# Kernel optimization log

Measured on AMD Instinct MI355X. Metric: run time of the kernel, lower is better.

The kernel has to match this reference:

```python
import jax, jax.numpy as jnp
import numpy as np

# Static graph-batch configuration (equal-size graphs so per-graph top-k is static)
B = 256          # number of graphs in the batch
N = 400          # nodes per graph
D = 256          # in_dim
DEG = 32         # average degree
E = B * N * DEG  # total edges
RATIO = 0.5
K = int(np.ceil(RATIO * N))  # nodes kept per graph by mytopk
NT = B * N


def setup_inputs() -> dict:
    key = jax.random.key(0)
    k1, k2, k3, k4 = jax.random.split(key, 4)
    feature = jax.random.normal(k1, (NT, D), dtype=jnp.float32)
    W = jax.random.normal(k2, (D, 1), dtype=jnp.float32) * (1.0 / np.sqrt(D))
    b = jnp.zeros((1,), dtype=jnp.float32)
    # edges stay within each graph: global id = graph_offset + local id
    g = jnp.repeat(jnp.arange(B, dtype=jnp.int32), N * DEG)  # [E] graph id per edge
    src = g * N + jax.random.randint(k3, (E,), 0, N, dtype=jnp.int32)
    dst = g * N + jax.random.randint(k4, (E,), 0, N, dtype=jnp.int32)
    return {"feature": feature, "W": W, "b": b, "src": src, "dst": dst}


def _forward(feature, W, b, src, dst):
    # --- GraphConv(in_dim, 1), norm='both' (dgl): h = D_in^-1/2 A D_out^-1/2 (X W) + b
    ones_e = jnp.ones((E,), dtype=feature.dtype)
    deg_out = jax.ops.segment_sum(ones_e, src, num_segments=NT)
    deg_in = jax.ops.segment_sum(ones_e, dst, num_segments=NT)
    norm_out = jnp.maximum(deg_out, 1.0) ** -0.5  # dgl clamps degree to min 1
    norm_in = jnp.maximum(deg_in, 1.0) ** -0.5
    h = (feature @ W) * norm_out[:, None]                      # [NT,1]
    agg = jax.ops.segment_sum(h[src], dst, num_segments=NT)    # [NT,1]
    score = (agg * norm_in[:, None] + b)[:, 0]                 # [NT]

    # --- mytopk: per-graph top-k node selection by score (descending)
    score2d = score.reshape(B, N)
    _, idx = jax.lax.top_k(score2d, K)                         # [B,K] local ids
    offsets = (jnp.arange(B, dtype=jnp.int32) * N)[:, None]
    perm = (idx.astype(jnp.int32) + offsets).reshape(-1)       # [B*K] global ids

    # complement nodes (mask trick in the original): ascending order per graph
    sel = jnp.zeros((NT,), dtype=bool).at[perm].set(True)
    sel2d = sel.reshape(B, N).astype(jnp.int32)
    order = jnp.argsort(sel2d, axis=1, stable=True)[:, : N - K]  # unselected first
    perm_com = (order.astype(jnp.int32) + offsets).reshape(-1)   # [B*(N-K)]

    # --- gated feature gathers
    feature_dis = feature[perm] * jnp.tanh(score[perm])[:, None]
    feature_com = feature[perm_com] * jnp.tanh(score[perm_com])[:, None]

    # --- subgraph structure as static-shape edge masks (dgl.node_subgraph keeps
    #     edges whose both endpoints are selected)
    e_dis_mask = sel[src] & sel[dst]
    e_com_mask = (~sel[src]) & (~sel[dst])

    score_soft = jax.nn.softmax(score, axis=0)  # Softmax(dim=0) over all nodes
    return feature_dis, feature_com, perm, perm_com, score_soft, e_dis_mask, e_com_mask


def reference(feature, W, b, src, dst):
    return _forward(feature, W, b, src, dst)
```

## Files before the change

kernel.cpp:

```cpp
#include <hip/hip_runtime.h>
#include <math.h>

#define B_    256
#define N_    400
#define D_    256
#define EPG_  12800
#define E_    3276800
#define NT_   102400
#define K_    200
#define NKC_  200

#define O_FDIS 0
#define O_FCOM 13107200
#define O_PERM 26214400
#define O_PCOM 26265600
#define O_SOFT 26316800
#define O_EDIS 26419200
#define O_ECOM 29696000

#define NEG_INF (-3.402823466e38f)

typedef float nfv4 __attribute__((ext_vector_type(4)));
static __device__ __forceinline__ void nt_store4(float4* p, float4 v) {
    nfv4 x; x.x = v.x; x.y = v.y; x.z = v.z; x.w = v.w;
    __builtin_nontemporal_store(x, (nfv4*)p);
}

__global__ __launch_bounds__(256) void k_h(const float* __restrict__ feat,
                                           const float* __restrict__ W,
                                           float* __restrict__ hraw,
                                           int* __restrict__ degz) {
    const int gid  = blockIdx.x * 256 + threadIdx.x;
    if (gid < 2 * NT_) degz[gid] = 0;
    const int gw   = gid >> 6;
    const int lane = threadIdx.x & 63;
    const float4 w4 = ((const float4*)W)[lane];
    const int r0 = gw * 4;
    const float4* fb = (const float4*)feat;
    float4 a0 = fb[(size_t)(r0    ) * 64 + lane];
    float4 a1 = fb[(size_t)(r0 + 1) * 64 + lane];
    float4 a2 = fb[(size_t)(r0 + 2) * 64 + lane];
    float4 a3 = fb[(size_t)(r0 + 3) * 64 + lane];
    float d0 = a0.x*w4.x + a0.y*w4.y + a0.z*w4.z + a0.w*w4.w;
    float d1 = a1.x*w4.x + a1.y*w4.y + a1.z*w4.z + a1.w*w4.w;
    float d2 = a2.x*w4.x + a2.y*w4.y + a2.z*w4.z + a2.w*w4.w;
    float d3 = a3.x*w4.x + a3.y*w4.y + a3.z*w4.z + a3.w*w4.w;
    #pragma unroll
    for (int off = 32; off > 0; off >>= 1) {
        d0 += __shfl_down(d0, off, 64);
        d1 += __shfl_down(d1, off, 64);
        d2 += __shfl_down(d2, off, 64);
        d3 += __shfl_down(d3, off, 64);
    }
    if (lane == 0) {
        hraw[r0    ] = d0;
        hraw[r0 + 1] = d1;
        hraw[r0 + 2] = d2;
        hraw[r0 + 3] = d3;
    }
}

__global__ __launch_bounds__(256) void k_deg(const int* __restrict__ src,
                                             const int* __restrict__ dst,
                                             int* __restrict__ dego,
                                             int* __restrict__ degi,
                                             float* __restrict__ aggz) {
    __shared__ int hp[8][N_];
    const int blk = blockIdx.x, tid = threadIdx.x, wave = tid >> 6;
    const int gid = blk * 256 + tid;
    if (gid < NT_) aggz[gid] = 0.0f;
    for (int t = tid; t < 8 * N_; t += 256) ((int*)hp)[t] = 0;
    __syncthreads();

    const int g = blk >> 2, nbase = g * N_;
    int* hw_o = hp[wave * 2 + 0];
    int* hw_i = hp[wave * 2 + 1];
    const int4* s4 = (const int4*)(src + blk * (EPG_ / 4));
    const int4* d4 = (const int4*)(dst + blk * (EPG_ / 4));
    for (int i = tid; i < EPG_ / 16; i += 256) {
        int4 s = s4[i]; int4 d = d4[i];
        atomicAdd(&hw_o[s.x - nbase], 1);
        atomicAdd(&hw_o[s.y - nbase], 1);
        atomicAdd(&hw_o[s.z - nbase], 1);
        atomicAdd(&hw_o[s.w - nbase], 1);
        atomicAdd(&hw_i[d.x - nbase], 1);
        atomicAdd(&hw_i[d.y - nbase], 1);
        atomicAdd(&hw_i[d.z - nbase], 1);
        atomicAdd(&hw_i[d.w - nbase], 1);
    }
    __syncthreads();
    for (int t = tid; t < N_; t += 256) {
        atomicAdd(&dego[nbase + t], hp[0][t] + hp[2][t] + hp[4][t] + hp[6][t]);
        atomicAdd(&degi[nbase + t], hp[1][t] + hp[3][t] + hp[5][t] + hp[7][t]);
    }
}

__global__ __launch_bounds__(256) void k_scat(const int* __restrict__ src,
                                              const int* __restrict__ dst,
                                              const float* __restrict__ hraw,
                                              const int* __restrict__ dego,
                                              float* __restrict__ agg) {
    __shared__ float hl[N_];
    __shared__ float sp[4][N_];
    const int blk = blockIdx.x, tid = threadIdx.x, wave = tid >> 6;
    const int g = blk >> 2, nbase = g * N_;
    for (int t = tid; t < N_; t += 256)
        hl[t] = hraw[nbase + t] * (1.0f / sqrtf(fmaxf((float)dego[nbase + t], 1.0f)));
    for (int t = tid; t < 4 * N_; t += 256) ((float*)sp)[t] = 0.0f;
    __syncthreads();

    float* spw = sp[wave];
    const int4* s4 = (const int4*)(src + blk * (EPG_ / 4));
    const int4* d4 = (const int4*)(dst + blk * (EPG_ / 4));
    for (int i = tid; i < EPG_ / 16; i += 256) {
        int4 s = s4[i]; int4 d = d4[i];
        atomicAdd(&spw[d.x - nbase], hl[s.x - nbase]);
        atomicAdd(&spw[d.y - nbase], hl[s.y - nbase]);
        atomicAdd(&spw[d.z - nbase], hl[s.z - nbase]);
        atomicAdd(&spw[d.w - nbase], hl[s.w - nbase]);
    }
    __syncthreads();
    for (int t = tid; t < N_; t += 256)
        atomicAdd(&agg[nbase + t], sp[0][t] + sp[1][t] + sp[2][t] + sp[3][t]);
}

__global__ __launch_bounds__(512) void k_top(float* __restrict__ sc,
                                             const int* __restrict__ degi,
                                             const float* __restrict__ bp,
                                             float* __restrict__ pm,
                                             float* __restrict__ ps,
                                             int* __restrict__ sel,
                                             int* __restrict__ orow,
                                             float* __restrict__ out) {
    __shared__ float scl[N_];
    __shared__ unsigned long long bmask[7];
    const int g = blockIdx.x, tid = threadIdx.x;
    const int wave = tid >> 6, lane = tid & 63;
    const int nbase = g * N_;

    const float bb = bp[0];
    if (tid < N_) {
        float v = sc[nbase + tid] * (1.0f / sqrtf(fmaxf((float)degi[nbase + tid], 1.0f))) + bb;
        sc[nbase + tid] = v;
        scl[tid] = v;
    }
    __syncthreads();

    bool selb = false;
    if (tid < 448) {
        float sreg[7];
        #pragma unroll
        for (int t = 0; t < 7; ++t) {
            const int j = t * 64 + lane;
            sreg[t] = (j < N_) ? scl[j] : NEG_INF;
        }
        const float v = (tid < N_) ? scl[tid] : NEG_INF;
        int rnk = 0;
        #pragma unroll
        for (int t = 0; t < 7; ++t) {
            #pragma unroll
            for (int l2 = 0; l2 < 64; ++l2) {
                const int j = t * 64 + l2;
                if (j < N_) {
                    const float u = __uint_as_float(
                        __builtin_amdgcn_readlane(__float_as_uint(sreg[t]), l2));
                    rnk += ((u > v) || (u == v && j < tid)) ? 1 : 0;
                }
            }
        }
        selb = (tid < N_) && (rnk < K_);
        if (tid < N_) sel[nbase + tid] = selb ? 1 : 0;
        if (selb) {
            orow[nbase + tid] = g * K_ + rnk;
            out[O_PERM + g * K_ + rnk] = (float)(nbase + tid);
        }
        unsigned long long bal = __ballot(selb);
        if (lane == 0) bmask[wave] = bal;
    }
    if (wave == 7) {
        float m = NEG_INF;
        for (int i = lane; i < N_; i += 64) m = fmaxf(m, scl[i]);
        #pragma unroll
        for (int o = 32; o > 0; o >>= 1) m = fmaxf(m, __shfl_xor(m, o, 64));
        float s = 0.0f;
        for (int i = lane; i < N_; i += 64) s += expf(scl[i] - m);
        #pragma unroll
        for (int o = 32; o > 0; o >>= 1) s += __shfl_xor(s, o, 64);
        if (lane == 0) { pm[g] = m; ps[g] = s; }
    }
    __syncthreads();

    if (tid < N_ && !selb) {
        int nsel = 0;
        #pragma unroll
        for (int w = 0; w < 7; ++w)
            if (w < wave) nsel += (int)__popcll(bmask[w]);
        nsel += (int)__popcll(bmask[wave] & ((1ull << lane) - 1ull));
        const int pos = tid - nsel;
        orow[nbase + tid] = B_ * K_ + g * NKC_ + pos;
        out[O_PCOM + g * NKC_ + pos] = (float)(nbase + tid);
    }
}

__global__ __launch_bounds__(256) void k_soft_comb(const float* pm, const float* ps, float* red2) {
    __shared__ float rm[256], rs[256];
    int tid = threadIdx.x;
    float m = pm[tid];
    rm[tid] = m; __syncthreads();
    for (int o = 128; o > 0; o >>= 1) { if (tid < o) rm[tid] = fmaxf(rm[tid], rm[tid + o]); __syncthreads(); }
    float M = rm[0]; __syncthreads();
    rs[tid] = ps[tid] * expf(m - M); __syncthreads();
    for (int o = 128; o > 0; o >>= 1) { if (tid < o) rs[tid] += rs[tid + o]; __syncthreads(); }
    if (tid == 0) { red2[0] = M; red2[1] = rs[0]; }
}

__global__ __launch_bounds__(256) void k_mask(const int* __restrict__ src,
                                              const int* __restrict__ dst,
                                              const int* __restrict__ sel,
                                              float* __restrict__ out) {
    const int i = blockIdx.x * 256 + threadIdx.x;
    int4 s = ((const int4*)src)[i];
    int4 d = ((const int4*)dst)[i];
    int a0 = sel[s.x], a1 = sel[s.y], a2 = sel[s.z], a3 = sel[s.w];
    int b0 = sel[d.x], b1 = sel[d.y], b2 = sel[d.z], b3 = sel[d.w];
    float4 mdis, mcom;
    mdis.x = (a0 & b0) ? 1.0f : 0.0f;  mcom.x = (a0 | b0) ? 0.0f : 1.0f;
    mdis.y = (a1 & b1) ? 1.0f : 0.0f;  mcom.y = (a1 | b1) ? 0.0f : 1.0f;
    mdis.z = (a2 & b2) ? 1.0f : 0.0f;  mcom.z = (a2 | b2) ? 0.0f : 1.0f;
    mdis.w = (a3 & b3) ? 1.0f : 0.0f;  mcom.w = (a3 | b3) ? 0.0f : 1.0f;
    nt_store4(((float4*)(out + O_EDIS)) + i, mdis);
    nt_store4(((float4*)(out + O_ECOM)) + i, mcom);
}

__global__ __launch_bounds__(256) void k_gather(const float* __restrict__ feat,
                                                const float* __restrict__ score,
                                                const int* __restrict__ orow,
                                                const float* __restrict__ red2,
                                                float* __restrict__ out) {
    const int gw   = (blockIdx.x * 256 + threadIdx.x) >> 6;
    const int lane = threadIdx.x & 63;
    const int n0 = gw * 4;
    const float4* fb = (const float4*)feat;
    float4 v0 = fb[(size_t)(n0    ) * 64 + lane];
    float4 v1 = fb[(size_t)(n0 + 1) * 64 + lane];
    float4 v2 = fb[(size_t)(n0 + 2) * 64 + lane];
    float4 v3 = fb[(size_t)(n0 + 3) * 64 + lane];
    float s0 = score[n0], s1 = score[n0 + 1], s2 = score[n0 + 2], s3 = score[n0 + 3];
    int   r0 = orow[n0],  r1 = orow[n0 + 1],  r2 = orow[n0 + 2],  r3 = orow[n0 + 3];
    float t0 = tanhf(s0), t1 = tanhf(s1), t2 = tanhf(s2), t3 = tanhf(s3);
    v0.x *= t0; v0.y *= t0; v0.z *= t0; v0.w *= t0;
    v1.x *= t1; v1.y *= t1; v1.z *= t1; v1.w *= t1;
    v2.x *= t2; v2.y *= t2; v2.z *= t2; v2.w *= t2;
    v3.x *= t3; v3.y *= t3; v3.z *= t3; v3.w *= t3;
    nt_store4(((float4*)(out + (size_t)r0 * D_)) + lane, v0);
    nt_store4(((float4*)(out + (size_t)r1 * D_)) + lane, v1);
    nt_store4(((float4*)(out + (size_t)r2 * D_)) + lane, v2);
    nt_store4(((float4*)(out + (size_t)r3 * D_)) + lane, v3);
    if (lane == 0) {
        float M = red2[0], S = red2[1];
        out[O_SOFT + n0    ] = expf(s0 - M) / S;
        out[O_SOFT + n0 + 1] = expf(s1 - M) / S;
        out[O_SOFT + n0 + 2] = expf(s2 - M) / S;
        out[O_SOFT + n0 + 3] = expf(s3 - M) / S;
    }
}

extern "C" void kernel_launch(void* const* d_in, const int* in_sizes, int n_in,
                              void* d_out, int out_size, void* d_ws, size_t ws_size,
                              hipStream_t stream) {
    const float* feat = (const float*)d_in[0];
    const float* W    = (const float*)d_in[1];
    const float* bp   = (const float*)d_in[2];
    const int*   src  = (const int*)d_in[3];
    const int*   dst  = (const int*)d_in[4];
    float* out = (float*)d_out;

    char* ws = (char*)d_ws;
    int*   dego  = (int*)  (ws + 0);
    int*   degi  = (int*)  (ws + 409600);
    float* agg   = (float*)(ws + 819200);
    float* hraw  = (float*)(ws + 1228800);
    float* pm    = (float*)(ws + 1638400);
    float* ps    = (float*)(ws + 1639424);
    float* red2  = (float*)(ws + 1640448);
    int*   orow  = (int*)  (ws + 0);
    int*   sel   = (int*)  (ws + 1228800);
    float* score = agg;

    k_h        <<<NT_ / 16,     256, 0, stream>>>(feat, W, hraw, dego);
    k_deg      <<<4 * B_,       256, 0, stream>>>(src, dst, dego, degi, agg);
    k_scat     <<<4 * B_,       256, 0, stream>>>(src, dst, hraw, dego, agg);
    k_top      <<<B_,           512, 0, stream>>>(score, degi, bp, pm, ps, sel, orow, out);
    k_soft_comb<<<1,            256, 0, stream>>>(pm, ps, red2);
    k_mask     <<<E_ / 4 / 256, 256, 0, stream>>>(src, dst, sel, out);
    k_gather   <<<NT_ / 16,     256, 0, stream>>>(feat, score, orow, red2, out);
}
```

Measured before the change: 293.8 us.

## Merge seven launches into four with partial-sum buffers instead of global atomics

Degree counting runs as extra blocks in the same launch as the feature-weight dot product. The edge mask and gather/softmax kernels are likewise merged into one launch split by block index. Global atomics and zero-initialisation are replaced by per-quarter partial degree and aggregate buffers, which later kernels sum. The single-block softmax combine kernel is removed: every gather block redundantly re-reduces the 256 per-graph max/sum pairs with an online-softmax shuffle. This cuts launch overhead and serialisation at the cost of extra workspace traffic and some redundant reduction work.

```diff
diff --git a/kernel.cpp b/kernel.cpp
--- a/kernel.cpp
+++ b/kernel.cpp
@@ -9,6 +9,8 @@
 #define NT_   102400
 #define K_    200
 #define NKC_  200
+#define QB_   1024
+#define EPQ_  3200
 
 #define O_FDIS 0
 #define O_FCOM 13107200
@@ -26,93 +28,92 @@
     __builtin_nontemporal_store(x, (nfv4*)p);
 }
 
-__global__ __launch_bounds__(256) void k_h(const float* __restrict__ feat,
+__global__ __launch_bounds__(256) void k_A(const float* __restrict__ feat,
                                            const float* __restrict__ W,
+                                           const int* __restrict__ src,
+                                           const int* __restrict__ dst,
                                            float* __restrict__ hraw,
-                                           int* __restrict__ degz) {
-    const int gid  = blockIdx.x * 256 + threadIdx.x;
-    if (gid < 2 * NT_) degz[gid] = 0;
-    const int gw   = gid >> 6;
-    const int lane = threadIdx.x & 63;
-    const float4 w4 = ((const float4*)W)[lane];
-    const int r0 = gw * 4;
-    const float4* fb = (const float4*)feat;
-    float4 a0 = fb[(size_t)(r0    ) * 64 + lane];
-    float4 a1 = fb[(size_t)(r0 + 1) * 64 + lane];
-    float4 a2 = fb[(size_t)(r0 + 2) * 64 + lane];
-    float4 a3 = fb[(size_t)(r0 + 3) * 64 + lane];
-    float d0 = a0.x*w4.x + a0.y*w4.y + a0.z*w4.z + a0.w*w4.w;
-    float d1 = a1.x*w4.x + a1.y*w4.y + a1.z*w4.z + a1.w*w4.w;
-    float d2 = a2.x*w4.x + a2.y*w4.y + a2.z*w4.z + a2.w*w4.w;
-    float d3 = a3.x*w4.x + a3.y*w4.y + a3.z*w4.z + a3.w*w4.w;
-    #pragma unroll
-    for (int off = 32; off > 0; off >>= 1) {
-        d0 += __shfl_down(d0, off, 64);
-        d1 += __shfl_down(d1, off, 64);
-        d2 += __shfl_down(d2, off, 64);
-        d3 += __shfl_down(d3, off, 64);
-    }
-    if (lane == 0) {
-        hraw[r0    ] = d0;
-        hraw[r0 + 1] = d1;
-        hraw[r0 + 2] = d2;
-        hraw[r0 + 3] = d3;
-    }
-}
-
-__global__ __launch_bounds__(256) void k_deg(const int* __restrict__ src,
-                                             const int* __restrict__ dst,
-                                             int* __restrict__ dego,
-                                             int* __restrict__ degi,
-                                             float* __restrict__ aggz) {
-    __shared__ int hp[8][N_];
-    const int blk = blockIdx.x, tid = threadIdx.x, wave = tid >> 6;
-    const int gid = blk * 256 + tid;
-    if (gid < NT_) aggz[gid] = 0.0f;
-    for (int t = tid; t < 8 * N_; t += 256) ((int*)hp)[t] = 0;
-    __syncthreads();
-
-    const int g = blk >> 2, nbase = g * N_;
-    int* hw_o = hp[wave * 2 + 0];
-    int* hw_i = hp[wave * 2 + 1];
-    const int4* s4 = (const int4*)(src + blk * (EPG_ / 4));
-    const int4* d4 = (const int4*)(dst + blk * (EPG_ / 4));
-    for (int i = tid; i < EPG_ / 16; i += 256) {
-        int4 s = s4[i]; int4 d = d4[i];
-        atomicAdd(&hw_o[s.x - nbase], 1);
-        atomicAdd(&hw_o[s.y - nbase], 1);
-        atomicAdd(&hw_o[s.z - nbase], 1);
-        atomicAdd(&hw_o[s.w - nbase], 1);
-        atomicAdd(&hw_i[d.x - nbase], 1);
-        atomicAdd(&hw_i[d.y - nbase], 1);
-        atomicAdd(&hw_i[d.z - nbase], 1);
-        atomicAdd(&hw_i[d.w - nbase], 1);
-    }
-    __syncthreads();
-    for (int t = tid; t < N_; t += 256) {
-        atomicAdd(&dego[nbase + t], hp[0][t] + hp[2][t] + hp[4][t] + hp[6][t]);
-        atomicAdd(&degi[nbase + t], hp[1][t] + hp[3][t] + hp[5][t] + hp[7][t]);
-    }
-}
-
-__global__ __launch_bounds__(256) void k_scat(const int* __restrict__ src,
-                                              const int* __restrict__ dst,
-                                              const float* __restrict__ hraw,
-                                              const int* __restrict__ dego,
-                                              float* __restrict__ agg) {
+                                           int* __restrict__ degp_o,
+                                           int* __restrict__ degp_i) {
+    const int bid = blockIdx.x, tid = threadIdx.x;
+    if (bid < NT_ / 16) {
+        const int gw   = (bid * 256 + tid) >> 6;
+        const int lane = tid & 63;
+        const float4 w4 = ((const float4*)W)[lane];
+        const int r0 = gw * 4;
+        const float4* fb = (const float4*)feat;
+        float4 a0 = fb[(size_t)(r0    ) * 64 + lane];
+        float4 a1 = fb[(size_t)(r0 + 1) * 64 + lane];
+        float4 a2 = fb[(size_t)(r0 + 2) * 64 + lane];
+        float4 a3 = fb[(size_t)(r0 + 3) * 64 + lane];
+        float d0 = a0.x*w4.x + a0.y*w4.y + a0.z*w4.z + a0.w*w4.w;
+        float d1 = a1.x*w4.x + a1.y*w4.y + a1.z*w4.z + a1.w*w4.w;
+        float d2 = a2.x*w4.x + a2.y*w4.y + a2.z*w4.z + a2.w*w4.w;
+        float d3 = a3.x*w4.x + a3.y*w4.y + a3.z*w4.z + a3.w*w4.w;
+        #pragma unroll
+        for (int off = 32; off > 0; off >>= 1) {
+            d0 += __shfl_down(d0, off, 64);
+            d1 += __shfl_down(d1, off, 64);
+            d2 += __shfl_down(d2, off, 64);
+            d3 += __shfl_down(d3, off, 64);
+        }
+        if (lane == 0) {
+            hraw[r0    ] = d0;
+            hraw[r0 + 1] = d1;
+            hraw[r0 + 2] = d2;
+            hraw[r0 + 3] = d3;
+        }
+    } else {
+        __shared__ int hp[8][N_];
+        const int qb = bid - NT_ / 16;
+        const int wave = tid >> 6;
+        const int nbase = (qb >> 2) * N_;
+        for (int t = tid; t < 8 * N_; t += 256) ((int*)hp)[t] = 0;
+        __syncthreads();
+        int* hw_o = hp[wave * 2 + 0];
+        int* hw_i = hp[wave * 2 + 1];
+        const int4* s4 = (const int4*)(src + qb * EPQ_);
+        const int4* d4 = (const int4*)(dst + qb * EPQ_);
+        for (int i = tid; i < EPQ_ / 4; i += 256) {
+            int4 s = s4[i]; int4 d = d4[i];
+            atomicAdd(&hw_o[s.x - nbase], 1);
+            atomicAdd(&hw_o[s.y - nbase], 1);
+            atomicAdd(&hw_o[s.z - nbase], 1);
+            atomicAdd(&hw_o[s.w - nbase], 1);
+            atomicAdd(&hw_i[d.x - nbase], 1);
+            atomicAdd(&hw_i[d.y - nbase], 1);
+            atomicAdd(&hw_i[d.z - nbase], 1);
+            atomicAdd(&hw_i[d.w - nbase], 1);
+        }
+        __syncthreads();
+        for (int t = tid; t < N_; t += 256) {
+            degp_o[qb * N_ + t] = hp[0][t] + hp[2][t] + hp[4][t] + hp[6][t];
+            degp_i[qb * N_ + t] = hp[1][t] + hp[3][t] + hp[5][t] + hp[7][t];
+        }
+    }
+}
+
+__global__ __launch_bounds__(256) void k_B(const int* __restrict__ src,
+                                           const int* __restrict__ dst,
+                                           const float* __restrict__ hraw,
+                                           const int* __restrict__ degp_o,
+                                           float* __restrict__ aggp) {
     __shared__ float hl[N_];
     __shared__ float sp[4][N_];
-    const int blk = blockIdx.x, tid = threadIdx.x, wave = tid >> 6;
-    const int g = blk >> 2, nbase = g * N_;
-    for (int t = tid; t < N_; t += 256)
-        hl[t] = hraw[nbase + t] * (1.0f / sqrtf(fmaxf((float)dego[nbase + t], 1.0f)));
+    const int qb = blockIdx.x, tid = threadIdx.x, wave = tid >> 6;
+    const int g = qb >> 2, nbase = g * N_, g4 = g * 4;
+    for (int t = tid; t < N_; t += 256) {
+        const int dsum = degp_o[(g4 + 0) * N_ + t] + degp_o[(g4 + 1) * N_ + t]
+                       + degp_o[(g4 + 2) * N_ + t] + degp_o[(g4 + 3) * N_ + t];
+        hl[t] = hraw[nbase + t] * (1.0f / sqrtf(fmaxf((float)dsum, 1.0f)));
+    }
     for (int t = tid; t < 4 * N_; t += 256) ((float*)sp)[t] = 0.0f;
     __syncthreads();
 
     float* spw = sp[wave];
-    const int4* s4 = (const int4*)(src + blk * (EPG_ / 4));
-    const int4* d4 = (const int4*)(dst + blk * (EPG_ / 4));
-    for (int i = tid; i < EPG_ / 16; i += 256) {
+    const int4* s4 = (const int4*)(src + qb * EPQ_);
+    const int4* d4 = (const int4*)(dst + qb * EPQ_);
+    for (int i = tid; i < EPQ_ / 4; i += 256) {
         int4 s = s4[i]; int4 d = d4[i];
         atomicAdd(&spw[d.x - nbase], hl[s.x - nbase]);
         atomicAdd(&spw[d.y - nbase], hl[s.y - nbase]);
@@ -121,27 +122,32 @@
     }
     __syncthreads();
     for (int t = tid; t < N_; t += 256)
-        atomicAdd(&agg[nbase + t], sp[0][t] + sp[1][t] + sp[2][t] + sp[3][t]);
-}
-
-__global__ __launch_bounds__(512) void k_top(float* __restrict__ sc,
-                                             const int* __restrict__ degi,
-                                             const float* __restrict__ bp,
-                                             float* __restrict__ pm,
-                                             float* __restrict__ ps,
-                                             int* __restrict__ sel,
-                                             int* __restrict__ orow,
-                                             float* __restrict__ out) {
+        aggp[qb * N_ + t] = sp[0][t] + sp[1][t] + sp[2][t] + sp[3][t];
+}
+
+__global__ __launch_bounds__(512) void k_C(const float* __restrict__ aggp,
+                                           const int* __restrict__ degp_i,
+                                           const float* __restrict__ bp,
+                                           float* __restrict__ score,
+                                           float* __restrict__ pm,
+                                           float* __restrict__ ps,
+                                           int* __restrict__ sel,
+                                           int* __restrict__ orow,
+                                           float* __restrict__ out) {
     __shared__ float scl[N_];
     __shared__ unsigned long long bmask[7];
     const int g = blockIdx.x, tid = threadIdx.x;
     const int wave = tid >> 6, lane = tid & 63;
-    const int nbase = g * N_;
+    const int nbase = g * N_, g4 = g * 4;
 
     const float bb = bp[0];
     if (tid < N_) {
-        float v = sc[nbase + tid] * (1.0f / sqrtf(fmaxf((float)degi[nbase + tid], 1.0f))) + bb;
-        sc[nbase + tid] = v;
+        const float a = aggp[(g4 + 0) * N_ + tid] + aggp[(g4 + 1) * N_ + tid]
+                      + aggp[(g4 + 2) * N_ + tid] + aggp[(g4 + 3) * N_ + tid];
+        const int dsum = degp_i[(g4 + 0) * N_ + tid] + degp_i[(g4 + 1) * N_ + tid]
+                       + degp_i[(g4 + 2) * N_ + tid] + degp_i[(g4 + 3) * N_ + tid];
+        const float v = a * (1.0f / sqrtf(fmaxf((float)dsum, 1.0f))) + bb;
+        score[nbase + tid] = v;
         scl[tid] = v;
     }
     __syncthreads();
@@ -202,66 +208,71 @@
     }
 }
 
-__global__ __launch_bounds__(256) void k_soft_comb(const float* pm, const float* ps, float* red2) {
-    __shared__ float rm[256], rs[256];
-    int tid = threadIdx.x;
-    float m = pm[tid];
-    rm[tid] = m; __syncthreads();
-    for (int o = 128; o > 0; o >>= 1) { if (tid < o) rm[tid] = fmaxf(rm[tid], rm[tid + o]); __syncthreads(); }
-    float M = rm[0]; __syncthreads();
-    rs[tid] = ps[tid] * expf(m - M); __syncthreads();
-    for (int o = 128; o > 0; o >>= 1) { if (tid < o) rs[tid] += rs[tid + o]; __syncthreads(); }
-    if (tid == 0) { red2[0] = M; red2[1] = rs[0]; }
-}
-
-__global__ __launch_bounds__(256) void k_mask(const int* __restrict__ src,
-                                              const int* __restrict__ dst,
-                                              const int* __restrict__ sel,
-                                              float* __restrict__ out) {
-    const int i = blockIdx.x * 256 + threadIdx.x;
-    int4 s = ((const int4*)src)[i];
-    int4 d = ((const int4*)dst)[i];
-    int a0 = sel[s.x], a1 = sel[s.y], a2 = sel[s.z], a3 = sel[s.w];
-    int b0 = sel[d.x], b1 = sel[d.y], b2 = sel[d.z], b3 = sel[d.w];
-    float4 mdis, mcom;
-    mdis.x = (a0 & b0) ? 1.0f : 0.0f;  mcom.x = (a0 | b0) ? 0.0f : 1.0f;
-    mdis.y = (a1 & b1) ? 1.0f : 0.0f;  mcom.y = (a1 | b1) ? 0.0f : 1.0f;
-    mdis.z = (a2 & b2) ? 1.0f : 0.0f;  mcom.z = (a2 | b2) ? 0.0f : 1.0f;
-    mdis.w = (a3 & b3) ? 1.0f : 0.0f;  mcom.w = (a3 | b3) ? 0.0f : 1.0f;
-    nt_store4(((float4*)(out + O_EDIS)) + i, mdis);
-    nt_store4(((float4*)(out + O_ECOM)) + i, mcom);
-}
-
-__global__ __launch_bounds__(256) void k_gather(const float* __restrict__ feat,
-                                                const float* __restrict__ score,
-                                                const int* __restrict__ orow,
-                                                const float* __restrict__ red2,
-                                                float* __restrict__ out) {
-    const int gw   = (blockIdx.x * 256 + threadIdx.x) >> 6;
-    const int lane = threadIdx.x & 63;
-    const int n0 = gw * 4;
-    const float4* fb = (const float4*)feat;
-    float4 v0 = fb[(size_t)(n0    ) * 64 + lane];
-    float4 v1 = fb[(size_t)(n0 + 1) * 64 + lane];
-    float4 v2 = fb[(size_t)(n0 + 2) * 64 + lane];
-    float4 v3 = fb[(size_t)(n0 + 3) * 64 + lane];
-    float s0 = score[n0], s1 = score[n0 + 1], s2 = score[n0 + 2], s3 = score[n0 + 3];
-    int   r0 = orow[n0],  r1 = orow[n0 + 1],  r2 = orow[n0 + 2],  r3 = orow[n0 + 3];
-    float t0 = tanhf(s0), t1 = tanhf(s1), t2 = tanhf(s2), t3 = tanhf(s3);
-    v0.x *= t0; v0.y *= t0; v0.z *= t0; v0.w *= t0;
-    v1.x *= t1; v1.y *= t1; v1.z *= t1; v1.w *= t1;
-    v2.x *= t2; v2.y *= t2; v2.z *= t2; v2.w *= t2;
-    v3.x *= t3; v3.y *= t3; v3.z *= t3; v3.w *= t3;
-    nt_store4(((float4*)(out + (size_t)r0 * D_)) + lane, v0);
-    nt_store4(((float4*)(out + (size_t)r1 * D_)) + lane, v1);
-    nt_store4(((float4*)(out + (size_t)r2 * D_)) + lane, v2);
-    nt_store4(((float4*)(out + (size_t)r3 * D_)) + lane, v3);
-    if (lane == 0) {
-        float M = red2[0], S = red2[1];
-        out[O_SOFT + n0    ] = expf(s0 - M) / S;
-        out[O_SOFT + n0 + 1] = expf(s1 - M) / S;
-        out[O_SOFT + n0 + 2] = expf(s2 - M) / S;
-        out[O_SOFT + n0 + 3] = expf(s3 - M) / S;
+__global__ __launch_bounds__(256) void k_D(const float* __restrict__ feat,
+                                           const float* __restrict__ score,
+                                           const int* __restrict__ orow,
+                                           const float* __restrict__ pm,
+                                           const float* __restrict__ ps,
+                                           const int* __restrict__ src,
+                                           const int* __restrict__ dst,
+                                           const int* __restrict__ sel,
+                                           float* __restrict__ out) {
+    const int bid = blockIdx.x, tid = threadIdx.x;
+    if (bid < NT_ / 16) {
+        __shared__ float sm[4], ss[4];
+        const int lane = tid & 63, wv = tid >> 6;
+        float m = pm[tid], s = ps[tid];
+        #pragma unroll
+        for (int o = 32; o > 0; o >>= 1) {
+            float mo = __shfl_xor(m, o, 64);
+            float so = __shfl_xor(s, o, 64);
+            float M2 = fmaxf(m, mo);
+            s = s * expf(m - M2) + so * expf(mo - M2);
+            m = M2;
+        }
+        if (lane == 0) { sm[wv] = m; ss[wv] = s; }
+        __syncthreads();
+        const float M = fmaxf(fmaxf(sm[0], sm[1]), fmaxf(sm[2], sm[3]));
+        const float S = ss[0] * expf(sm[0] - M) + ss[1] * expf(sm[1] - M)
+                      + ss[2] * expf(sm[2] - M) + ss[3] * expf(sm[3] - M);
+
+        const int gw = (bid * 256 + tid) >> 6;
+        const int n0 = gw * 4;
+        const float4* fb = (const float4*)feat;
+        float4 v0 = fb[(size_t)(n0    ) * 64 + lane];
+        float4 v1 = fb[(size_t)(n0 + 1) * 64 + lane];
+        float4 v2 = fb[(size_t)(n0 + 2) * 64 + lane];
+        float4 v3 = fb[(size_t)(n0 + 3) * 64 + lane];
+        float s0 = score[n0], s1 = score[n0 + 1], s2 = score[n0 + 2], s3 = score[n0 + 3];
+        int   r0 = orow[n0],  r1 = orow[n0 + 1],  r2 = orow[n0 + 2],  r3 = orow[n0 + 3];
+        float t0 = tanhf(s0), t1 = tanhf(s1), t2 = tanhf(s2), t3 = tanhf(s3);
+        v0.x *= t0; v0.y *= t0; v0.z *= t0; v0.w *= t0;
+        v1.x *= t1; v1.y *= t1; v1.z *= t1; v1.w *= t1;
+        v2.x *= t2; v2.y *= t2; v2.z *= t2; v2.w *= t2;
+        v3.x *= t3; v3.y *= t3; v3.z *= t3; v3.w *= t3;
+        nt_store4(((float4*)(out + (size_t)r0 * D_)) + lane, v0);
+        nt_store4(((float4*)(out + (size_t)r1 * D_)) + lane, v1);
+        nt_store4(((float4*)(out + (size_t)r2 * D_)) + lane, v2);
+        nt_store4(((float4*)(out + (size_t)r3 * D_)) + lane, v3);
+        if (lane == 0) {
+            out[O_SOFT + n0    ] = expf(s0 - M) / S;
+            out[O_SOFT + n0 + 1] = expf(s1 - M) / S;
+            out[O_SOFT + n0 + 2] = expf(s2 - M) / S;
+            out[O_SOFT + n0 + 3] = expf(s3 - M) / S;
+        }
+    } else {
+        const int i = (bid - NT_ / 16) * 256 + tid;
+        int4 s = ((const int4*)src)[i];
+        int4 d = ((const int4*)dst)[i];
+        int a0 = sel[s.x], a1 = sel[s.y], a2 = sel[s.z], a3 = sel[s.w];
+        int b0 = sel[d.x], b1 = sel[d.y], b2 = sel[d.z], b3 = sel[d.w];
+        float4 mdis, mcom;
+        mdis.x = (a0 & b0) ? 1.0f : 0.0f;  mcom.x = (a0 | b0) ? 0.0f : 1.0f;
+        mdis.y = (a1 & b1) ? 1.0f : 0.0f;  mcom.y = (a1 | b1) ? 0.0f : 1.0f;
+        mdis.z = (a2 & b2) ? 1.0f : 0.0f;  mcom.z = (a2 | b2) ? 0.0f : 1.0f;
+        mdis.w = (a3 & b3) ? 1.0f : 0.0f;  mcom.w = (a3 | b3) ? 0.0f : 1.0f;
+        nt_store4(((float4*)(out + O_EDIS)) + i, mdis);
+        nt_store4(((float4*)(out + O_ECOM)) + i, mcom);
     }
 }
 
@@ -276,22 +287,19 @@
     float* out = (float*)d_out;
 
     char* ws = (char*)d_ws;
-    int*   dego  = (int*)  (ws + 0);
-    int*   degi  = (int*)  (ws + 409600);
-    float* agg   = (float*)(ws + 819200);
-    float* hraw  = (float*)(ws + 1228800);
-    float* pm    = (float*)(ws + 1638400);
-    float* ps    = (float*)(ws + 1639424);
-    float* red2  = (float*)(ws + 1640448);
-    int*   orow  = (int*)  (ws + 0);
-    int*   sel   = (int*)  (ws + 1228800);
-    float* score = agg;
-
-    k_h        <<<NT_ / 16,     256, 0, stream>>>(feat, W, hraw, dego);
-    k_deg      <<<4 * B_,       256, 0, stream>>>(src, dst, dego, degi, agg);
-    k_scat     <<<4 * B_,       256, 0, stream>>>(src, dst, hraw, dego, agg);
-    k_top      <<<B_,           512, 0, stream>>>(score, degi, bp, pm, ps, sel, orow, out);
-    k_soft_comb<<<1,            256, 0, stream>>>(pm, ps, red2);
-    k_mask     <<<E_ / 4 / 256, 256, 0, stream>>>(src, dst, sel, out);
-    k_gather   <<<NT_ / 16,     256, 0, stream>>>(feat, score, orow, red2, out);
-}
+    float* hraw   = (float*)(ws + 0);
+    int*   degp_o = (int*)  (ws + 409600);
+    int*   degp_i = (int*)  (ws + 2048000);
+    float* aggp   = (float*)(ws + 3686400);
+    float* score  = (float*)(ws + 5324800);
+    int*   sel    = (int*)  (ws + 5734400);
+    int*   orow   = (int*)  (ws + 6144000);
+    float* pm     = (float*)(ws + 6553600);
+    float* ps     = (float*)(ws + 6554624);
+
+    k_A<<<NT_ / 16 + QB_,  256, 0, stream>>>(feat, W, src, dst, hraw, degp_o, degp_i);
+    k_B<<<QB_,             256, 0, stream>>>(src, dst, hraw, degp_o, aggp);
+    k_C<<<B_,              512, 0, stream>>>(aggp, degp_i, bp, score, pm, ps, sel, orow, out);
+    k_D<<<NT_ / 16 + E_ / 4 / 256, 256, 0, stream>>>(feat, score, orow, pm, ps,
+                                                     src, dst, sel, out);
+}
```

Result: no change. 289.2 us (-1.5%).
